# Kernel tuning notes

Hardware: AMD Instinct MI355X
Metric: run time of the kernel (lower is better)

Reference implementation:

```python
import jax, jax.numpy as jnp
import numpy as np
from jax import lax

INF = 1e4          # 'infinite' distance for chamfer transform
THETA0 = 3.0       # boundary weight decay
K_CHAMFER = 24     # exp(-24/3)~3e-4: distances beyond this are negligible
SQ2 = 1.4142135


def setup_inputs() -> dict:
    key = jax.random.key(0)
    k1, k2 = jax.random.split(key)
    inputs = jax.random.normal(k1, (32, 1, 512, 512), jnp.float32)
    targets = (jax.random.uniform(k2, (32, 1, 512, 512)) < 0.3).astype(jnp.float32)
    alpha = jnp.float32(0.25)   # config.FOCAL_ALPHA, learnable
    gamma = jnp.float32(3.0)    # config.FOCAL_GAMMA, learnable
    return {"inputs": inputs, "targets": targets, "alpha": alpha, "gamma": gamma}


def _boundary_weight(t):
    """t: (B,H,W) binary mask -> boundary-distance weight exp(-d/theta0)+0.1.
    Faithful GPU-friendly replacement for cv2 findContours/drawContours(th=3)
    + distanceTransform(L2, 3): morphological external gradient, dilated once
    (3px band), then truncated chamfer distance transform."""
    B, H, W = t.shape
    tp = jnp.pad(t, ((0, 0), (1, 1), (1, 1)))  # pad 0 so border object pixels count as edge
    eroded = lax.reduce_window(tp, jnp.inf, lax.min, (1, 3, 3), (1, 1, 1), 'VALID')
    edge = t * (1.0 - eroded)                  # contour pixels (thickness 1)
    ep = jnp.pad(edge, ((0, 0), (1, 1), (1, 1)))
    bmask = lax.reduce_window(ep, -jnp.inf, lax.max, (1, 3, 3), (1, 1, 1), 'VALID')  # thickness 3

    d = jnp.where(bmask > 0.5, 0.0, INF)
    offs = [(-1, -1, SQ2), (-1, 0, 1.0), (-1, 1, SQ2), (0, -1, 1.0),
            (0, 1, 1.0), (1, -1, SQ2), (1, 0, 1.0), (1, 1, SQ2)]

    def shift(x, di, dj):
        xp = jnp.pad(x, ((0, 0), (max(di, 0), max(-di, 0)), (max(dj, 0), max(-dj, 0))),
                     constant_values=INF)
        return xp[:, max(-di, 0):max(-di, 0) + H, max(-dj, 0):max(-dj, 0) + W]

    def step(dc, _):
        nd = dc
        for di, dj, c in offs:
            nd = jnp.minimum(nd, shift(dc, di, dj) + c)
        return nd, None

    d, _ = lax.scan(step, d, None, length=K_CHAMFER)
    return jnp.exp(-jnp.minimum(d, INF) / THETA0) + 0.1


def reference(inputs, targets, alpha, gamma):
    probs = jax.nn.sigmoid(inputs)
    smooth = 1e-6
    eps = 1e-7

    # --- dice (smp binary, from_logits, global dims=(0,2)) ---
    inter = jnp.sum(probs * targets)
    card = jnp.sum(probs) + jnp.sum(targets)
    dice_score = (2.0 * inter + smooth) / jnp.maximum(card + smooth, eps)
    dice = jnp.where(jnp.sum(targets) > 0, 1.0 - dice_score, 0.0)

    # --- adaptive focal ---
    a = jnp.clip(alpha, 0.1, 0.9)
    g = jnp.clip(gamma, 1.0, 5.0)
    st = targets * 0.95 + 0.025  # label smoothing
    bce_el = st * jax.nn.softplus(-inputs) + (1.0 - st) * jax.nn.softplus(inputs)
    p_t = st * probs + (1.0 - st) * (1.0 - probs)
    a_t = st * a + (1.0 - st) * (1.0 - a)
    focal = jnp.mean(a_t * (1.0 - p_t) ** g * bce_el)

    # --- BCEWithLogits, pos_weight=7 ---
    bce = jnp.mean(7.0 * targets * jax.nn.softplus(-inputs)
                   + (1.0 - targets) * jax.nn.softplus(inputs))

    # --- dynamic tversky, class_weight=3 ---
    pos_ratio = jnp.mean(targets)
    da = 0.7 * (1.0 + pos_ratio)
    db = 0.3 * (2.0 - pos_ratio)
    tp = inter
    fn = jnp.sum(targets * (1.0 - probs))
    fp = jnp.sum((1.0 - targets) * probs) * 3.0
    tversky = 1.0 - (tp + smooth) / (tp + da * fn + db * fp + smooth)

    # --- boundary loss (preds detached in original) ---
    t2 = targets[:, 0]
    w = _boundary_weight(t2)
    p = jnp.clip(lax.stop_gradient(probs[:, 0]), 1e-7, 1.0 - 1e-7)
    bnd_bce = -(t2 * jnp.log(p) + (1.0 - t2) * jnp.log1p(-p))
    boundary = jnp.mean(jnp.mean(bnd_bce * w, axis=(1, 2)))

    return 0.35 * dice + 0.25 * focal + 0.15 * bce + 0.15 * tversky + 0.1 * boundary
```

## Files before the change

### kernel.cpp

```cpp
#include <hip/hip_runtime.h>

typedef unsigned long long u64;
typedef unsigned int u32;

#define HH 512
#define WW 512
#define BATCH 32
#define NPIX (BATCH*HH*WW)
#define NQ (NPIX/4)
#define NWORDS (NPIX/64)
#define WPI (HH*WW/64)
#define WPR (WW/64)

#define PS_BLOCKS (BATCH*16)

#define SEARCH_BLOCKS 1024
#define MAIN_BLOCKS 2048
#define TOTAL_BLOCKS (SEARCH_BLOCKS + MAIN_BLOCKS)
#define MAIN_TT (MAIN_BLOCKS*256)

#define WINMASK ((((1ULL<<49)-1)) << 8)

#define WS_PART   0
#define WS_TBITS  262144
#define WS_BMBITS 1310720

__device__ __forceinline__ float hw_exp2(float x) { return __builtin_amdgcn_exp2f(x); }
__device__ __forceinline__ float hw_log2(float x) { return __builtin_amdgcn_logf(x); }

__global__ __launch_bounds__(256) void pack_stencil_kernel(
        const float4* __restrict__ t4, u64* __restrict__ tbits,
        u64* __restrict__ bmbits) {
    __shared__ u64 lw[36][9];

    const int blk = blockIdx.x;
    const int img = blk >> 4;
    const int strip = blk & 15;
    const int row0 = strip * 32;

    unsigned char* lb = (unsigned char*)lw;
    #pragma unroll
    for (int it = 0; it < 9; ++it) {
        int i = it * 256 + threadIdx.x;
        int r = i >> 6, c = i & 63;
        int gy = row0 - 2 + r;
        unsigned b = 0;
        if (gy >= 0 && gy < HH) {
            int base = img * (HH*WW/4) + gy * (WW/4) + c * 2;
            float4 lo = t4[base], hi = t4[base + 1];
            b =  (lo.x > 0.5f)       | ((lo.y > 0.5f) << 1)
              | ((lo.z > 0.5f) << 2) | ((lo.w > 0.5f) << 3)
              | ((hi.x > 0.5f) << 4) | ((hi.y > 0.5f) << 5)
              | ((hi.z > 0.5f) << 6) | ((hi.w > 0.5f) << 7);
        }
        lb[r * 72 + c] = (unsigned char)b;
    }
    __syncthreads();

    const int r  = threadIdx.x >> 3;
    const int wc = threadIdx.x & 7;

    u64 w[5][5];
    #pragma unroll
    for (int dr = 0; dr < 5; ++dr)
        #pragma unroll
        for (int dc = 0; dc < 5; ++dc) {
            int cc = wc + dc - 2;
            w[dr][dc] = (cc >= 0 && cc < 8) ? lw[r + dr][cc] : 0ULL;
        }

    u64 ha[5][3];
    #pragma unroll
    for (int rr = 0; rr < 5; ++rr)
        #pragma unroll
        for (int j = 0; j < 3; ++j) {
            u64 C = w[rr][j + 1], L = w[rr][j], R = w[rr][j + 2];
            ha[rr][j] = ((C << 1) | (L >> 63)) & C & ((C >> 1) | (R << 63));
        }

    u64 eg[3][3];
    #pragma unroll
    for (int i = 0; i < 3; ++i)
        #pragma unroll
        for (int j = 0; j < 3; ++j) {
            u64 er = ha[i][j] & ha[i + 1][j] & ha[i + 2][j];
            eg[i][j] = w[i + 1][j + 1] & ~er;
        }

    u64 out = 0ULL;
    #pragma unroll
    for (int i = 0; i < 3; ++i) {
        u64 E = eg[i][1], L = eg[i][0], R = eg[i][2];
        out |= ((E << 1) | (L >> 63)) | E | ((E >> 1) | (R << 63));
    }

    int gw = img * WPI + (row0 + r) * WPR + wc;
    tbits[gw]  = w[2][2];
    bmbits[gw] = out;
}

__device__ __forceinline__ int rowscan(const u64* __restrict__ row, int x0) {
    int s = x0 - 32;
    int wi = s >> 6;
    int sh = s & 63;
    u64 lo = (wi >= 0 && wi < WPR) ? row[wi] : 0ULL;
    u64 hi = ((wi + 1) < WPR) ? row[wi + 1] : 0ULL;
    u64 win = sh ? ((lo >> sh) | (hi << (64 - sh))) : lo;
    win &= WINMASK;
    u64 left = win << 32;
    u64 right = win >> 32;
    int dl = left ? (__builtin_clzll(left) + 1) : 99;
    int dr = right ? __builtin_ctzll(right) : 99;
    return dl < dr ? dl : dr;
}

__device__ __forceinline__ float search_weight(const u64* __restrict__ img, int pix) {
    const float L2E = 1.44269504f;
    int x0 = pix & (WW - 1);
    int y0 = (pix >> 9) & (HH - 1);
    float best = 1e9f;
    for (int ady = 0; ady <= 24; ++ady) {
        if ((float)ady >= best) break;
        int hd = 99;
        int yU = y0 - ady;
        if (yU >= 0) hd = rowscan(img + yU * WPR, x0);
        int yD = y0 + ady;
        if (ady > 0 && yD < HH) {
            int h2 = rowscan(img + yD * WPR, x0);
            hd = h2 < hd ? h2 : hd;
        }
        if (hd <= 24) {
            float h = (float)hd, ay = (float)ady;
            float mx = fmaxf(h, ay), mn = fminf(h, ay);
            best = fminf(best, mx + 0.4142135f * mn);
        }
    }
    return (best < 1e8f) ? (hw_exp2(best * (-L2E / 3.0f)) + 0.1f) : 0.1f;
}

__global__ __launch_bounds__(256, 4) void fused_kernel(
        const float4* __restrict__ x4, const float* __restrict__ x,
        const u64* __restrict__ tbits, const u64* __restrict__ bmbits,
        const float* __restrict__ alpha_p, const float* __restrict__ gamma_p,
        double* __restrict__ partials) {
    __shared__ double red[4][6];

    const float LOGCLIP = 16.11809565f;
    const float L2E = 1.44269504f;
    const float LN2 = 0.69314718f;

    double d_p = 0.0, d_t = 0.0, d_pt = 0.0, d_f = 0.0, d_b = 0.0, d_bnd = 0.0;

    if (blockIdx.x < SEARCH_BLOCKS) {
        int h = blockIdx.x * 256 + threadIdx.x;
        int wi = h >> 1;
        int sh32 = (h & 1) * 32;
        u32 m = ~(u32)(bmbits[wi] >> sh32);
        u32 twh = (u32)(tbits[wi] >> sh32);
        const u64* img = bmbits + (wi >> 12) * WPI;
        int pixbase = wi * 64 + sh32;
        float acc = 0.f;
        while (m) {
            int b = __builtin_ctz(m);
            m &= m - 1;
            int pix = pixbase + b;
            float xv = x[pix];
            int tb = (int)((twh >> b) & 1u);
            float ax = fabsf(xv);
            float e = hw_exp2(ax * -L2E);
            float l1pe = hw_log2(1.0f + e) * LN2;
            float sp_neg = fmaxf(-xv, 0.0f) + l1pe;
            float sp = tb ? sp_neg : (sp_neg + xv);
            float bnd = fminf(sp, LOGCLIP);
            acc += bnd * search_weight(img, pix);
        }
        d_bnd = (double)acc;
    } else {
        const float a = fminf(fmaxf(alpha_p[0], 0.1f), 0.9f);
        const float one_m_a = 1.0f - a;
        const float g = fminf(fmaxf(gamma_p[0], 1.0f), 5.0f);
        const float gr = rintf(g);
        const bool gint = (g == gr);
        const int gi = (int)gr;

        const int q0 = (blockIdx.x - SEARCH_BLOCKS) * 256 + threadIdx.x;
        float4 xv[4];
        u32 tn[4], bn[4];
        #pragma unroll
        for (int j = 0; j < 4; ++j) {
            int q = q0 + j * MAIN_TT;
            xv[j] = x4[q];
            int sh = (q & 15) * 4;
            tn[j] = (u32)((tbits[q >> 4]  >> sh) & 0xfULL);
            bn[j] = (u32)((bmbits[q >> 4] >> sh) & 0xfULL);
        }

        float s_p = 0.f, s_pt = 0.f, s_f = 0.f, s_b = 0.f, s_bnd = 0.f;
        int c_t = 0;

        #pragma unroll
        for (int j = 0; j < 4; ++j) {
            float xs[4] = {xv[j].x, xv[j].y, xv[j].z, xv[j].w};
            #pragma unroll
            for (int k = 0; k < 4; ++k) {
                float xvv = xs[k];
                int tb = (int)((tn[j] >> k) & 1u);
                int bm = (int)((bn[j] >> k) & 1u);

                float ax = fabsf(xvv);
                float e  = hw_exp2(ax * -L2E);
                float rc = __builtin_amdgcn_rcpf(1.0f + e);
                float p  = (xvv >= 0.0f) ? rc : e * rc;
                float l1pe = hw_log2(1.0f + e) * LN2;
                float sp_neg = fmaxf(-xvv, 0.0f) + l1pe;
                float sp_pos = sp_neg + xvv;

                float bce_el = sp_neg + (tb ? 0.025f : 0.975f) * xvv;
                float q95 = 0.95f * p;
                float u   = tb ? (0.975f - q95) : (0.025f + q95);
                float a_t = tb ? a : one_m_a;
                float pw;
                if (gint) {
                    float u2 = u * u;
                    pw = (gi == 1) ? u : (gi == 2) ? u2 : (gi == 3) ? u2 * u
                       : (gi == 4) ? u2 * u2 : u2 * u2 * u;
                } else {
                    pw = hw_exp2(g * hw_log2(u));
                }
                float focal_el = a_t * pw * bce_el;

                float bce2 = tb ? 7.0f * sp_neg : sp_pos;
                float bnd  = fminf(tb ? sp_neg : sp_pos, LOGCLIP);

                s_p   += p;
                c_t   += tb;
                s_pt  += tb ? p : 0.0f;
                s_f   += focal_el;
                s_b   += bce2;
                s_bnd += bm ? bnd : 0.0f;
            }
        }
        d_p = s_p; d_t = (double)c_t; d_pt = s_pt; d_f = s_f; d_b = s_b;
        d_bnd = (double)s_bnd * 1.1;
    }

    #pragma unroll
    for (int off = 32; off > 0; off >>= 1) {
        d_p   += __shfl_down(d_p, off);
        d_t   += __shfl_down(d_t, off);
        d_pt  += __shfl_down(d_pt, off);
        d_f   += __shfl_down(d_f, off);
        d_b   += __shfl_down(d_b, off);
        d_bnd += __shfl_down(d_bnd, off);
    }
    int lane = threadIdx.x & 63, wid = threadIdx.x >> 6;
    if (lane == 0) {
        red[wid][0] = d_p;  red[wid][1] = d_t;  red[wid][2] = d_pt;
        red[wid][3] = d_f;  red[wid][4] = d_b;  red[wid][5] = d_bnd;
    }
    __syncthreads();
    if (threadIdx.x == 0) {
        #pragma unroll
        for (int i = 0; i < 6; ++i)
            partials[blockIdx.x * 6 + i] = red[0][i] + red[1][i] + red[2][i] + red[3][i];
    }
}

__global__ __launch_bounds__(256) void reduce_kernel(const double* __restrict__ partials,
                                                     float* __restrict__ out) {
    double s[6] = {0, 0, 0, 0, 0, 0};
    for (int b = threadIdx.x; b < TOTAL_BLOCKS; b += 256)
        #pragma unroll
        for (int i = 0; i < 6; ++i) s[i] += partials[b * 6 + i];

    #pragma unroll
    for (int off = 32; off > 0; off >>= 1)
        #pragma unroll
        for (int i = 0; i < 6; ++i) s[i] += __shfl_down(s[i], off);

    __shared__ double red[4][6];
    int lane = threadIdx.x & 63, wid = threadIdx.x >> 6;
    if (lane == 0)
        #pragma unroll
        for (int i = 0; i < 6; ++i) red[wid][i] = s[i];
    __syncthreads();

    if (threadIdx.x == 0) {
        double S_p = red[0][0] + red[1][0] + red[2][0] + red[3][0];
        double S_t = red[0][1] + red[1][1] + red[2][1] + red[3][1];
        double S_pt = red[0][2] + red[1][2] + red[2][2] + red[3][2];
        double S_f = red[0][3] + red[1][3] + red[2][3] + red[3][3];
        double S_b = red[0][4] + red[1][4] + red[2][4] + red[3][4];
        double S_bnd = red[0][5] + red[1][5] + red[2][5] + red[3][5];
        const double N = (double)NPIX;
        double inter = S_pt;
        double card = S_p + S_t;
        double dice_score = (2.0 * inter + 1e-6) / fmax(card + 1e-6, 1e-7);
        double dice = (S_t > 0.0) ? (1.0 - dice_score) : 0.0;
        double focal = S_f / N;
        double bce = S_b / N;
        double pos_ratio = S_t / N;
        double da = 0.7 * (1.0 + pos_ratio);
        double db = 0.3 * (2.0 - pos_ratio);
        double fn = S_t - S_pt;
        double fp = (S_p - S_pt) * 3.0;
        double tversky = 1.0 - (S_pt + 1e-6) / (S_pt + da * fn + db * fp + 1e-6);
        double bnd = S_bnd / N;
        out[0] = (float)(0.35 * dice + 0.25 * focal + 0.15 * bce + 0.15 * tversky + 0.1 * bnd);
    }
}

extern "C" void kernel_launch(void* const* d_in, const int* in_sizes, int n_in,
                              void* d_out, int out_size, void* d_ws, size_t ws_size,
                              hipStream_t stream) {
    const float* inputs  = (const float*)d_in[0];
    const float* targets = (const float*)d_in[1];
    const float* alpha_p = (const float*)d_in[2];
    const float* gamma_p = (const float*)d_in[3];
    float* out = (float*)d_out;

    char* ws = (char*)d_ws;
    double* partials = (double*)(ws + WS_PART);
    u64*    tbits    = (u64*)(ws + WS_TBITS);
    u64*    bmbits   = (u64*)(ws + WS_BMBITS);

    pack_stencil_kernel<<<PS_BLOCKS, 256, 0, stream>>>(
        (const float4*)targets, tbits, bmbits);

    fused_kernel<<<TOTAL_BLOCKS, 256, 0, stream>>>(
        (const float4*)inputs, inputs, tbits, bmbits, alpha_p, gamma_p, partials);

    reduce_kernel<<<1, 256, 0, stream>>>(partials, out);
}
```

Baseline: 42.82 us.

## Stage 49-row bitmask window in LDS per image row for boundary search

The boundary-distance search now runs one block per image row (BATCH*HH blocks). Each block loads the 49 surrounding bitmask rows into shared memory with zero padding, and every thread serves two pixels of that row. The row scans read from LDS without bounds checks instead of from scattered global loads. The cost is far more blocks (16384 search blocks), per-block sync and load overhead, and lanes that idle when their pixels are inside the band. The workspace offsets grow to fit the larger partials array.

Result: slower. 105.2 us (+145.7%).

```diff
diff --git a/kernel.cpp b/kernel.cpp
--- a/kernel.cpp
+++ b/kernel.cpp
@@ -14,16 +14,16 @@
 
 #define PS_BLOCKS (BATCH*16)
 
-#define SEARCH_BLOCKS 1024
+#define SEARCH_ROWBLOCKS (BATCH*HH)
 #define MAIN_BLOCKS 2048
-#define TOTAL_BLOCKS (SEARCH_BLOCKS + MAIN_BLOCKS)
+#define TOTAL_BLOCKS (SEARCH_ROWBLOCKS + MAIN_BLOCKS)
 #define MAIN_TT (MAIN_BLOCKS*256)
 
 #define WINMASK ((((1ULL<<49)-1)) << 8)
 
 #define WS_PART   0
-#define WS_TBITS  262144
-#define WS_BMBITS 1310720
+#define WS_TBITS  1048576
+#define WS_BMBITS 2097152
 
 __device__ __forceinline__ float hw_exp2(float x) { return __builtin_amdgcn_exp2f(x); }
 __device__ __forceinline__ float hw_log2(float x) { return __builtin_amdgcn_logf(x); }
@@ -99,12 +99,12 @@
     bmbits[gw] = out;
 }
 
-__device__ __forceinline__ int rowscan(const u64* __restrict__ row, int x0) {
+__device__ __forceinline__ int rowscan_lds(const u64* row, int x0) {
     int s = x0 - 32;
     int wi = s >> 6;
     int sh = s & 63;
-    u64 lo = (wi >= 0 && wi < WPR) ? row[wi] : 0ULL;
-    u64 hi = ((wi + 1) < WPR) ? row[wi + 1] : 0ULL;
+    u64 lo = row[wi + 1];
+    u64 hi = row[wi + 2];
     u64 win = sh ? ((lo >> sh) | (hi << (64 - sh))) : lo;
     win &= WINMASK;
     u64 left = win << 32;
@@ -114,35 +114,12 @@
     return dl < dr ? dl : dr;
 }
 
-__device__ __forceinline__ float search_weight(const u64* __restrict__ img, int pix) {
-    const float L2E = 1.44269504f;
-    int x0 = pix & (WW - 1);
-    int y0 = (pix >> 9) & (HH - 1);
-    float best = 1e9f;
-    for (int ady = 0; ady <= 24; ++ady) {
-        if ((float)ady >= best) break;
-        int hd = 99;
-        int yU = y0 - ady;
-        if (yU >= 0) hd = rowscan(img + yU * WPR, x0);
-        int yD = y0 + ady;
-        if (ady > 0 && yD < HH) {
-            int h2 = rowscan(img + yD * WPR, x0);
-            hd = h2 < hd ? h2 : hd;
-        }
-        if (hd <= 24) {
-            float h = (float)hd, ay = (float)ady;
-            float mx = fmaxf(h, ay), mn = fminf(h, ay);
-            best = fminf(best, mx + 0.4142135f * mn);
-        }
-    }
-    return (best < 1e8f) ? (hw_exp2(best * (-L2E / 3.0f)) + 0.1f) : 0.1f;
-}
-
 __global__ __launch_bounds__(256, 4) void fused_kernel(
         const float4* __restrict__ x4, const float* __restrict__ x,
         const u64* __restrict__ tbits, const u64* __restrict__ bmbits,
         const float* __restrict__ alpha_p, const float* __restrict__ gamma_p,
         double* __restrict__ partials) {
+    __shared__ u64 rows[49][10];
     __shared__ double red[4][6];
 
     const float LOGCLIP = 16.11809565f;
@@ -151,28 +128,53 @@
 
     double d_p = 0.0, d_t = 0.0, d_pt = 0.0, d_f = 0.0, d_b = 0.0, d_bnd = 0.0;
 
-    if (blockIdx.x < SEARCH_BLOCKS) {
-        int h = blockIdx.x * 256 + threadIdx.x;
-        int wi = h >> 1;
-        int sh32 = (h & 1) * 32;
-        u32 m = ~(u32)(bmbits[wi] >> sh32);
-        u32 twh = (u32)(tbits[wi] >> sh32);
-        const u64* img = bmbits + (wi >> 12) * WPI;
-        int pixbase = wi * 64 + sh32;
+    if (blockIdx.x < SEARCH_ROWBLOCKS) {
+        const int img = blockIdx.x >> 9;
+        const int y0 = blockIdx.x & (HH - 1);
+        const u64* ibase = bmbits + img * WPI;
+
+        for (int i = threadIdx.x; i < 49 * 10; i += 256) {
+            int r = i / 10, c = i % 10;
+            int gy = y0 - 24 + r;
+            u64 v = 0ULL;
+            if (c >= 1 && c <= 8 && gy >= 0 && gy < HH) v = ibase[gy * WPR + (c - 1)];
+            rows[r][c] = v;
+        }
+        __syncthreads();
+
         float acc = 0.f;
-        while (m) {
-            int b = __builtin_ctz(m);
-            m &= m - 1;
-            int pix = pixbase + b;
-            float xv = x[pix];
-            int tb = (int)((twh >> b) & 1u);
-            float ax = fabsf(xv);
-            float e = hw_exp2(ax * -L2E);
-            float l1pe = hw_log2(1.0f + e) * LN2;
-            float sp_neg = fmaxf(-xv, 0.0f) + l1pe;
-            float sp = tb ? sp_neg : (sp_neg + xv);
-            float bnd = fminf(sp, LOGCLIP);
-            acc += bnd * search_weight(img, pix);
+        #pragma unroll
+        for (int j = 0; j < 2; ++j) {
+            int x0p = threadIdx.x + j * 256;
+            int bm = (int)((rows[24][1 + (x0p >> 6)] >> (x0p & 63)) & 1ULL);
+            if (!bm) {
+                int pix = img * (HH * WW) + y0 * WW + x0p;
+                float xv = x[pix];
+                int tb = (int)((tbits[pix >> 6] >> (pix & 63)) & 1ULL);
+                float ax = fabsf(xv);
+                float e = hw_exp2(ax * -L2E);
+                float l1pe = hw_log2(1.0f + e) * LN2;
+                float sp_neg = fmaxf(-xv, 0.0f) + l1pe;
+                float sp = tb ? sp_neg : (sp_neg + xv);
+                float bnd = fminf(sp, LOGCLIP);
+
+                float best = 1e9f;
+                #pragma unroll 1
+                for (int ady = 0; ady <= 24; ++ady) {
+                    if ((float)ady >= best) break;
+                    int hd = rowscan_lds(rows[24 - ady], x0p);
+                    if (ady > 0) {
+                        int h2 = rowscan_lds(rows[24 + ady], x0p);
+                        hd = h2 < hd ? h2 : hd;
+                    }
+                    if (hd <= 24) {
+                        float fh = (float)hd, fa = (float)ady;
+                        best = fminf(best, fmaxf(fh, fa) + 0.4142135f * fminf(fh, fa));
+                    }
+                }
+                float wgt = (best < 1e8f) ? (hw_exp2(best * (-L2E / 3.0f)) + 0.1f) : 0.1f;
+                acc += bnd * wgt;
+            }
         }
         d_bnd = (double)acc;
     } else {
@@ -183,7 +185,7 @@
         const bool gint = (g == gr);
         const int gi = (int)gr;
 
-        const int q0 = (blockIdx.x - SEARCH_BLOCKS) * 256 + threadIdx.x;
+        const int q0 = (blockIdx.x - SEARCH_ROWBLOCKS) * 256 + threadIdx.x;
         float4 xv[4];
         u32 tn[4], bn[4];
         #pragma unroll
```

## Precompute transposed per-pixel horizontal boundary distance field for search

Applied to the files above, without the earlier changes.

Adds a kernel that computes, for every pixel, the horizontal distance (up to 24) to the nearest boundary-band pixel and stores it as bytes in a column-major (transposed) layout. The per-pixel boundary weight search then reads 64 contiguous bytes of that column and takes a branchless min over the vertical window, replacing up to 49 row-scans with bit manipulation and early exit. This trades an extra kernel launch and about 9 MB of workspace writes and reads for a fixed, less divergent inner loop. The scattered column reads per pixel may add memory traffic.

New measurement: 71.94 us. 1.68x slower.

```diff
diff --git a/kernel.cpp b/kernel.cpp
--- a/kernel.cpp
+++ b/kernel.cpp
@@ -13,6 +13,7 @@
 #define WPR (WW/64)
 
 #define PS_BLOCKS (BATCH*16)
+#define HF_BLOCKS (BATCH*64)
 
 #define SEARCH_BLOCKS 1024
 #define MAIN_BLOCKS 2048
@@ -21,9 +22,13 @@
 
 #define WINMASK ((((1ULL<<49)-1)) << 8)
 
+#define HT_STRIDE 576
+#define HT_IMG (WW*HT_STRIDE)
+
 #define WS_PART   0
 #define WS_TBITS  262144
 #define WS_BMBITS 1310720
+#define WS_HT     2359296
 
 __device__ __forceinline__ float hw_exp2(float x) { return __builtin_amdgcn_exp2f(x); }
 __device__ __forceinline__ float hw_log2(float x) { return __builtin_amdgcn_logf(x); }
@@ -99,40 +104,78 @@
     bmbits[gw] = out;
 }
 
-__device__ __forceinline__ int rowscan(const u64* __restrict__ row, int x0) {
-    int s = x0 - 32;
-    int wi = s >> 6;
-    int sh = s & 63;
-    u64 lo = (wi >= 0 && wi < WPR) ? row[wi] : 0ULL;
-    u64 hi = ((wi + 1) < WPR) ? row[wi + 1] : 0ULL;
-    u64 win = sh ? ((lo >> sh) | (hi << (64 - sh))) : lo;
-    win &= WINMASK;
-    u64 left = win << 32;
-    u64 right = win >> 32;
-    int dl = left ? (__builtin_clzll(left) + 1) : 99;
-    int dr = right ? __builtin_ctzll(right) : 99;
-    return dl < dr ? dl : dr;
-}
-
-__device__ __forceinline__ float search_weight(const u64* __restrict__ img, int pix) {
+__global__ __launch_bounds__(256) void hfield_kernel(const u64* __restrict__ bmbits,
+                                                     unsigned char* __restrict__ hT) {
+    __shared__ unsigned char tile[64][68];
+
+    const int blk = blockIdx.x;
+    const int img = blk >> 6;
+    const int ty = (blk >> 3) & 7;
+    const int tx = blk & 7;
+    const int Y0 = ty * 64, X0 = tx * 64;
+
+    {
+        const int r = threadIdx.x >> 2;
+        const int q = threadIdx.x & 3;
+        const u64* rowp = bmbits + img * WPI + (Y0 + r) * WPR;
+        u64 wl = (tx >= 1) ? rowp[tx - 1] : 0ULL;
+        u64 wm = rowp[tx];
+        u64 wr = (tx <= 6) ? rowp[tx + 1] : 0ULL;
+        #pragma unroll
+        for (int j = 0; j < 16; ++j) {
+            int p = q * 16 + j;
+            int s = p + 32;
+            int wi = s >> 6, sh = s & 63;
+            u64 lo = wi ? wm : wl;
+            u64 hi = wi ? wr : wm;
+            u64 win = sh ? ((lo >> sh) | (hi << (64 - sh))) : lo;
+            win &= WINMASK;
+            u64 left = win << 32, right = win >> 32;
+            int dl = left ? (__builtin_clzll(left) + 1) : 99;
+            int dr = right ? __builtin_ctzll(right) : 99;
+            tile[r][p] = (unsigned char)(dl < dr ? dl : dr);
+        }
+    }
+    __syncthreads();
+    {
+        const int c = threadIdx.x >> 2;
+        const int yc = (threadIdx.x & 3) * 16;
+        u32 v0 = 0, v1 = 0, v2 = 0, v3 = 0;
+        #pragma unroll
+        for (int b = 0; b < 4; ++b) {
+            v0 |= (u32)tile[yc + b][c]      << (8 * b);
+            v1 |= (u32)tile[yc + 4 + b][c]  << (8 * b);
+            v2 |= (u32)tile[yc + 8 + b][c]  << (8 * b);
+            v3 |= (u32)tile[yc + 12 + b][c] << (8 * b);
+        }
+        uint4 o; o.x = v0; o.y = v1; o.z = v2; o.w = v3;
+        *(uint4*)(hT + (size_t)img * HT_IMG + (size_t)(X0 + c) * HT_STRIDE + Y0 + yc) = o;
+    }
+}
+
+__device__ __forceinline__ float search_weight_hT(const unsigned char* __restrict__ col,
+                                                  int y0) {
     const float L2E = 1.44269504f;
-    int x0 = pix & (WW - 1);
-    int y0 = (pix >> 9) & (HH - 1);
+    int ylo = y0 - 24; ylo = ylo < 0 ? 0 : ylo;
+    int yhi = y0 + 24; yhi = yhi > (HH - 1) ? (HH - 1) : yhi;
+    int b16 = ylo & ~15;
+    const uint4* p = (const uint4*)(col + b16);
+    uint4 r0 = p[0], r1 = p[1], r2 = p[2], r3 = p[3];
+    u32 ws[16] = {r0.x, r0.y, r0.z, r0.w, r1.x, r1.y, r1.z, r1.w,
+                  r2.x, r2.y, r2.z, r2.w, r3.x, r3.y, r3.z, r3.w};
     float best = 1e9f;
-    for (int ady = 0; ady <= 24; ++ady) {
-        if ((float)ady >= best) break;
-        int hd = 99;
-        int yU = y0 - ady;
-        if (yU >= 0) hd = rowscan(img + yU * WPR, x0);
-        int yD = y0 + ady;
-        if (ady > 0 && yD < HH) {
-            int h2 = rowscan(img + yD * WPR, x0);
-            hd = h2 < hd ? h2 : hd;
-        }
-        if (hd <= 24) {
-            float h = (float)hd, ay = (float)ady;
-            float mx = fmaxf(h, ay), mn = fminf(h, ay);
-            best = fminf(best, mx + 0.4142135f * mn);
+    #pragma unroll
+    for (int w = 0; w < 16; ++w) {
+        u32 v = ws[w];
+        #pragma unroll
+        for (int b = 0; b < 4; ++b) {
+            int y = b16 + w * 4 + b;
+            int h = (int)((v >> (8 * b)) & 255u);
+            int ady = y - y0; ady = ady < 0 ? -ady : ady;
+            bool ok = (y >= ylo) && (y <= yhi) && (h <= 24);
+            float fh = (float)h, fa = (float)ady;
+            float cost = fmaxf(fh, fa) + 0.4142135f * fminf(fh, fa);
+            best = fminf(best, ok ? cost : 1e9f);
         }
     }
     return (best < 1e8f) ? (hw_exp2(best * (-L2E / 3.0f)) + 0.1f) : 0.1f;
@@ -141,6 +184,7 @@
 __global__ __launch_bounds__(256, 4) void fused_kernel(
         const float4* __restrict__ x4, const float* __restrict__ x,
         const u64* __restrict__ tbits, const u64* __restrict__ bmbits,
+        const unsigned char* __restrict__ hT,
         const float* __restrict__ alpha_p, const float* __restrict__ gamma_p,
         double* __restrict__ partials) {
     __shared__ double red[4][6];
@@ -152,12 +196,12 @@
     double d_p = 0.0, d_t = 0.0, d_pt = 0.0, d_f = 0.0, d_b = 0.0, d_bnd = 0.0;
 
     if (blockIdx.x < SEARCH_BLOCKS) {
-        int h = blockIdx.x * 256 + threadIdx.x;
-        int wi = h >> 1;
-        int sh32 = (h & 1) * 32;
+        int hw_id = blockIdx.x * 256 + threadIdx.x;
+        int wi = hw_id >> 1;
+        int sh32 = (hw_id & 1) * 32;
         u32 m = ~(u32)(bmbits[wi] >> sh32);
         u32 twh = (u32)(tbits[wi] >> sh32);
-        const u64* img = bmbits + (wi >> 12) * WPI;
+        const unsigned char* imgT = hT + (size_t)(wi >> 12) * HT_IMG;
         int pixbase = wi * 64 + sh32;
         float acc = 0.f;
         while (m) {
@@ -172,7 +216,8 @@
             float sp_neg = fmaxf(-xv, 0.0f) + l1pe;
             float sp = tb ? sp_neg : (sp_neg + xv);
             float bnd = fminf(sp, LOGCLIP);
-            acc += bnd * search_weight(img, pix);
+            const unsigned char* col = imgT + (size_t)(pix & (WW - 1)) * HT_STRIDE;
+            acc += bnd * search_weight_hT(col, (pix >> 9) & (HH - 1));
         }
         d_bnd = (double)acc;
     } else {
@@ -320,15 +365,18 @@
     float* out = (float*)d_out;
 
     char* ws = (char*)d_ws;
-    double* partials = (double*)(ws + WS_PART);
-    u64*    tbits    = (u64*)(ws + WS_TBITS);
-    u64*    bmbits   = (u64*)(ws + WS_BMBITS);
+    double* partials       = (double*)(ws + WS_PART);
+    u64*    tbits          = (u64*)(ws + WS_TBITS);
+    u64*    bmbits         = (u64*)(ws + WS_BMBITS);
+    unsigned char* hT      = (unsigned char*)(ws + WS_HT);
 
     pack_stencil_kernel<<<PS_BLOCKS, 256, 0, stream>>>(
         (const float4*)targets, tbits, bmbits);
 
+    hfield_kernel<<<HF_BLOCKS, 256, 0, stream>>>(bmbits, hT);
+
     fused_kernel<<<TOTAL_BLOCKS, 256, 0, stream>>>(
-        (const float4*)inputs, inputs, tbits, bmbits, alpha_p, gamma_p, partials);
+        (const float4*)inputs, inputs, tbits, bmbits, hT, alpha_p, gamma_p, partials);
 
     reduce_kernel<<<1, 256, 0, stream>>>(partials, out);
 }
```
